# Optimization experiments

Measured on AMD Instinct MI355X. Metric: run time of the kernel, lower is better.

Reference implementation:

```python
import jax, jax.numpy as jnp
import numpy as np

B, S, D, H = 2, 2048, 1024, 16
HD = D // H  # head_dim = 64
SCALE = HD ** -0.5


def setup_inputs() -> dict:
    key = jax.random.key(0)
    k1, k2, k3 = jax.random.split(key, 3)
    src = jax.random.normal(k1, (B, S, D), dtype=jnp.float32)
    w_qkv = jax.random.normal(k2, (D, 3 * D), dtype=jnp.float32) * (D ** -0.5)
    b_qkv = jax.random.normal(k3, (3 * D,), dtype=jnp.float32) * 0.02
    return {"src": src, "w_qkv": w_qkv, "b_qkv": b_qkv}


def reference(src, w_qkv, b_qkv):
    # qkv projection: [B,S,3D]
    qkv = src @ w_qkv + b_qkv
    q, k, v = jnp.split(qkv, 3, axis=-1)
    # [B,S,D] -> [B,H,S,HD]
    def heads(x):
        return x.reshape(B, S, H, HD).transpose(0, 2, 1, 3)
    q, k, v = heads(q), heads(k), heads(v)
    # scaled dot-product attention (note: original scales AFTER q@k.T)
    attn = jnp.einsum('bhqd,bhkd->bhqk', q, k) * SCALE
    attn = jax.nn.softmax(attn, axis=-1)
    out = jnp.einsum('bhqk,bhkd->bhqd', attn, v)  # [B,H,S,HD]
    return out.transpose(0, 2, 1, 3).reshape(B, S, D)
```

## Files before the change

### kernel.cpp

```cpp
#include <hip/hip_runtime.h>
#include <hip/hip_bf16.h>

typedef short short8 __attribute__((ext_vector_type(8)));
typedef float f32x4 __attribute__((ext_vector_type(4)));
typedef float f32x16 __attribute__((ext_vector_type(16)));
typedef __hip_bfloat16 bf16;


__device__ __forceinline__ void glds16(const void* g, void* l) {
  __builtin_amdgcn_global_load_lds((const __attribute__((address_space(1))) unsigned int*)g,
                                   (__attribute__((address_space(3))) unsigned int*)l, 16, 0, 0);
}

__device__ __forceinline__ uint pk2(float a, float b) {
  union { bf16 h2[2]; uint u; } pk;
  pk.h2[0] = __float2bfloat16(a);
  pk.h2[1] = __float2bfloat16(b);
  return pk.u;
}

__global__ __launch_bounds__(256) void prep_kernel(const float4* __restrict__ in,
                                                   bf16* __restrict__ src_bf,
                                                   const float* __restrict__ w,
                                                   bf16* __restrict__ wt) {
  __shared__ float tile[32][33];
  const int bid = blockIdx.x;
  if (bid < 4096) {
    int i = bid * 256 + threadIdx.x;
    float4 v = in[i];
    union { bf16 h[4]; uint2 u; } pk;
    pk.h[0] = __float2bfloat16(v.x);
    pk.h[1] = __float2bfloat16(v.y);
    pk.h[2] = __float2bfloat16(v.z);
    pk.h[3] = __float2bfloat16(v.w);
    *(uint2*)(src_bf + (size_t)i * 4) = pk.u;
  } else {
    int id = bid - 4096;
    int x0 = (id % 96) * 32;
    int y0 = (id / 96) * 32;
    int tx = threadIdx.x & 31, ty = threadIdx.x >> 5;
#pragma unroll
    for (int i = 0; i < 4; i++) {
      int y = ty + i * 8;
      tile[y][tx] = w[(size_t)(y0 + y) * 3072 + x0 + tx];
    }
    __syncthreads();
#pragma unroll
    for (int i = 0; i < 4; i++) {
      int y = ty + i * 8;
      wt[(size_t)(x0 + y) * 1024 + y0 + tx] = __float2bfloat16(tile[tx][y]);
    }
  }
}

__global__ __launch_bounds__(256) void qkv_gemm_kernel(
    const bf16* __restrict__ A, const bf16* __restrict__ Bt,
    const float* __restrict__ bias,
    bf16* __restrict__ q_ws, bf16* __restrict__ k_ws, bf16* __restrict__ vt_ws) {
  __shared__ alignas(16) char AB[32768];
  const int tid = threadIdx.x;
  const int lane = tid & 63, wid = tid >> 6;
  const int lr = lane & 15, lg = lane >> 4;
  const int wm = wid >> 1, wn = wid & 1;
  const int m0 = blockIdx.x * 128, n0 = blockIdx.y * 128;

  const f32x4 z4 = {0.f, 0.f, 0.f, 0.f};
  f32x4 acc[4][4];
#pragma unroll
  for (int m = 0; m < 4; m++)
#pragma unroll
    for (int n = 0; n < 4; n++) acc[m][n] = z4;

  const int srow = lane >> 3;
  const int sseg = (lane & 7) ^ srow;
  const char* Ag = (const char*)A + (size_t)(m0 + wid * 32 + srow) * 2048 + sseg * 16;
  const char* Bg = (const char*)Bt + (size_t)(n0 + wid * 32 + srow) * 2048 + sseg * 16;
  char* Al = AB + wid * 4096;
  char* Bl = AB + 16384 + wid * 4096;
  const int xora = (lr & 7) << 4;

  for (int kt = 0; kt < 16; kt++) {
    __syncthreads();
#pragma unroll
    for (int c = 0; c < 4; c++) {
      glds16(Ag + (size_t)kt * 128 + c * 16384, Al + c * 1024);
      glds16(Bg + (size_t)kt * 128 + c * 16384, Bl + c * 1024);
    }
    asm volatile("s_waitcnt vmcnt(0)" ::: "memory");
    __syncthreads();
#pragma unroll
    for (int g = 0; g < 2; g++) {
      short8 af[4], bfr[4];
#pragma unroll
      for (int m = 0; m < 4; m++)
        af[m] = *(const short8*)(AB + (wm * 64 + m * 16 + lr) * 128 +
                                 ((g * 64 + lg * 16) ^ xora));
#pragma unroll
      for (int n = 0; n < 4; n++)
        bfr[n] = *(const short8*)(AB + 16384 + (wn * 64 + n * 16 + lr) * 128 +
                                  ((g * 64 + lg * 16) ^ xora));
#pragma unroll
      for (int m = 0; m < 4; m++)
#pragma unroll
        for (int n = 0; n < 4; n++)
          acc[m][n] = __builtin_amdgcn_mfma_f32_16x16x32_bf16(af[m], bfr[n], acc[m][n], 0, 0, 0);
    }
  }

  const int which = n0 >> 10;
#pragma unroll
  for (int m = 0; m < 4; m++) {
    int row = m0 + wm * 64 + m * 16 + lg * 4;
    int b = row >> 11;
    int ss0 = row & 2047;
#pragma unroll
    for (int n = 0; n < 4; n++) {
      int col = n0 + wn * 64 + n * 16 + lr;
      int d = col & 1023;
      int h = d >> 6, hd = d & 63;
      size_t bh = (size_t)(b * 16 + h);
      float bv = bias[col];
      if (which == 2) {
        union { bf16 h4[4]; uint2 u; } pk;
#pragma unroll
        for (int r = 0; r < 4; r++) pk.h4[r] = __float2bfloat16(acc[m][n][r] + bv);
        *(uint2*)&vt_ws[(bh * 64 + hd) * 2048 + ss0] = pk.u;
      } else {
        bf16* dst = (which == 0) ? q_ws : k_ws;
#pragma unroll
        for (int r = 0; r < 4; r++)
          dst[(bh * 2048 + (ss0 + r)) * 64 + hd] = __float2bfloat16(acc[m][n][r] + bv);
      }
    }
  }
}

__global__ __launch_bounds__(512) void attn6_kernel(
    const bf16* __restrict__ q_ws, const bf16* __restrict__ k_ws,
    const bf16* __restrict__ vt_ws, float* __restrict__ out) {
  __shared__ alignas(16) char smem[65536];
  const int tid = threadIdx.x;
  const int lane = tid & 63, wid = tid >> 6;
  const int lq = lane & 31, hi = lane >> 5;
  const int hi16 = hi * 16;
  const int xorv = (lq & 7) << 4;
  const float scale_l2e = 0.125f * 1.44269504088896f;

  const int f = blockIdx.x;
  const int bh = (f & 7) * 4 + ((f >> 3) & 3);
  const int qb = f >> 5;
  const int b = bh >> 4, h = bh & 15;
  const int q0 = qb * 256 + wid * 32;

  short8 qf[4];
  {
    const bf16* qrow = q_ws + ((size_t)bh * 2048 + q0 + lq) * 64;
#pragma unroll
    for (int s = 0; s < 4; s++) qf[s] = *(const short8*)(qrow + s * 16 + hi * 8);
  }

  const int l8 = lane >> 3;
  const int segk = (lane & 7) ^ l8;
  const char* kgl = (const char*)k_ws + (size_t)bh * 262144 +
                    (size_t)(wid * 16 + l8) * 128 + segk * 16;
  const int l16 = lane >> 4;
  const int d0v = (wid * 2 + 0) * 4 + l16;
  const int d1v = (wid * 2 + 1) * 4 + l16;
  const char* vg0 = (const char*)vt_ws + (size_t)bh * 262144 + (size_t)d0v * 4096 +
                    (((lane & 15) ^ (d0v & 15)) << 4);
  const char* vg1 = (const char*)vt_ws + (size_t)bh * 262144 + (size_t)d1v * 4096 +
                    (((lane & 15) ^ (d1v & 15)) << 4);

  f32x16 o0a, o0b, o1a, o1b, lacc;
#pragma unroll
  for (int r = 0; r < 16; r++) {
    o0a[r] = 0.f; o0b[r] = 0.f; o1a[r] = 0.f; o1b[r] = 0.f; lacc[r] = 0.f;
  }

  glds16(kgl, smem + wid * 2048);
  glds16(kgl + 1024, smem + wid * 2048 + 1024);
  glds16(vg0, smem + 32768 + wid * 2048);
  glds16(vg1, smem + 32768 + wid * 2048 + 1024);
  asm volatile("s_waitcnt vmcnt(0)" ::: "memory");
  __builtin_amdgcn_s_barrier();

  for (int kt = 0; kt < 16; ++kt) {
    const int kb_off = (kt & 1) * 16384;
    const int vb_off = 32768 + (kt & 1) * 16384;
    if (kt + 1 < 16) {
      const int nb = ((kt + 1) & 1) * 16384;
      glds16(kgl + (size_t)(kt + 1) * 16384, smem + nb + wid * 2048);
      glds16(kgl + (size_t)(kt + 1) * 16384 + 1024, smem + nb + wid * 2048 + 1024);
      glds16(vg0 + (size_t)(kt + 1) * 256, smem + 32768 + nb + wid * 2048);
      glds16(vg1 + (size_t)(kt + 1) * 256, smem + 32768 + nb + wid * 2048 + 1024);
    }

    f32x16 s0, s1, s2, s3;
#pragma unroll
    for (int r = 0; r < 16; r++) { s0[r] = 0.f; s1[r] = 0.f; s2[r] = 0.f; s3[r] = 0.f; }
#pragma unroll
    for (int st = 0; st < 4; st++) {
      const int doff = (st * 32 + hi16) ^ xorv;
      short8 ka = *(const short8*)(smem + kb_off + lq * 128 + doff);
      short8 kb = *(const short8*)(smem + kb_off + (lq + 32) * 128 + doff);
      short8 kc = *(const short8*)(smem + kb_off + (lq + 64) * 128 + doff);
      short8 kd = *(const short8*)(smem + kb_off + (lq + 96) * 128 + doff);
      __builtin_amdgcn_s_setprio(1);
      s0 = __builtin_amdgcn_mfma_f32_32x32x16_bf16(ka, qf[st], s0, 0, 0, 0);
      s1 = __builtin_amdgcn_mfma_f32_32x32x16_bf16(kb, qf[st], s1, 0, 0, 0);
      s2 = __builtin_amdgcn_mfma_f32_32x32x16_bf16(kc, qf[st], s2, 0, 0, 0);
      s3 = __builtin_amdgcn_mfma_f32_32x32x16_bf16(kd, qf[st], s3, 0, 0, 0);
      __builtin_amdgcn_s_setprio(0);
    }

#pragma unroll
    for (int r = 0; r < 16; r++) {
      s0[r] = __builtin_amdgcn_exp2f(s0[r] * scale_l2e);
      s1[r] = __builtin_amdgcn_exp2f(s1[r] * scale_l2e);
      s2[r] = __builtin_amdgcn_exp2f(s2[r] * scale_l2e);
      s3[r] = __builtin_amdgcn_exp2f(s3[r] * scale_l2e);
    }
#pragma unroll
    for (int r = 0; r < 16; r++)
      lacc[r] += (s0[r] + s1[r]) + (s2[r] + s3[r]);

#define PV_KB(S, KB, OA, OB)                                                     \
  {                                                                              \
    uint w0 = pk2(S[0], S[1]), w1 = pk2(S[2], S[3]);                             \
    uint w2 = pk2(S[4], S[5]), w3 = pk2(S[6], S[7]);                             \
    uint w4 = pk2(S[8], S[9]), w5 = pk2(S[10], S[11]);                           \
    uint w6 = pk2(S[12], S[13]), w7 = pk2(S[14], S[15]);                         \
    uint r0 = (uint)__shfl_xor((int)(hi ? w0 : w2), 32);                         \
    uint r1 = (uint)__shfl_xor((int)(hi ? w1 : w3), 32);                         \
    uint r2 = (uint)__shfl_xor((int)(hi ? w4 : w6), 32);                         \
    uint r3 = (uint)__shfl_xor((int)(hi ? w5 : w7), 32);                         \
    union { uint u[4]; short8 s8; } ua, ub;                                      \
    ua.u[0] = hi ? r0 : w0; ua.u[1] = hi ? r1 : w1;                              \
    ua.u[2] = hi ? w2 : r0; ua.u[3] = hi ? w3 : r1;                              \
    ub.u[0] = hi ? r2 : w4; ub.u[1] = hi ? r3 : w5;                              \
    ub.u[2] = hi ? w6 : r2; ub.u[3] = hi ? w7 : r3;                              \
    const int c0 = (((KB) * 4 + hi) ^ (lq & 15)) << 4;                           \
    const int c1 = (((KB) * 4 + 2 + hi) ^ (lq & 15)) << 4;                       \
    short8 va0 = *(const short8*)(smem + vb_off + lq * 256 + c0);                \
    short8 va1 = *(const short8*)(smem + vb_off + (lq + 32) * 256 + c0);         \
    short8 vb0 = *(const short8*)(smem + vb_off + lq * 256 + c1);                \
    short8 vb1 = *(const short8*)(smem + vb_off + (lq + 32) * 256 + c1);         \
    __builtin_amdgcn_s_setprio(1);                                               \
    OA = __builtin_amdgcn_mfma_f32_32x32x16_bf16(va0, ua.s8, OA, 0, 0, 0);       \
    OB = __builtin_amdgcn_mfma_f32_32x32x16_bf16(va1, ua.s8, OB, 0, 0, 0);       \
    OA = __builtin_amdgcn_mfma_f32_32x32x16_bf16(vb0, ub.s8, OA, 0, 0, 0);       \
    OB = __builtin_amdgcn_mfma_f32_32x32x16_bf16(vb1, ub.s8, OB, 0, 0, 0);       \
    __builtin_amdgcn_s_setprio(0);                                               \
  }
    PV_KB(s0, 0, o0a, o1a)
    PV_KB(s1, 1, o0b, o1b)
    PV_KB(s2, 2, o0a, o1a)
    PV_KB(s3, 3, o0b, o1b)
#undef PV_KB

    if (kt < 15) {
      asm volatile("s_waitcnt vmcnt(0)" ::: "memory");
      __builtin_amdgcn_s_barrier();
    }
  }
  __syncthreads();

  float l;
  {
    float sm[8];
#pragma unroll
    for (int i = 0; i < 8; i++) sm[i] = lacc[i] + lacc[i + 8];
#pragma unroll
    for (int i = 0; i < 4; i++) sm[i] += sm[i + 4];
    l = (sm[0] + sm[1]) + (sm[2] + sm[3]);
    l += __shfl_xor(l, 32);
  }
  f32x16 o0, o1;
#pragma unroll
  for (int r = 0; r < 16; r++) { o0[r] = o0a[r] + o0b[r]; o1[r] = o1a[r] + o1b[r]; }
  float* ep = (float*)(smem) + wid * 1024;
  const float invl = 1.f / l;
  const int eq = lane >> 1, eds = lane & 1;
  float* obase = out + ((size_t)b * 2048 + qb * 256 + wid * 32 + eq) * 1024 +
                 h * 64 + eds * 16;
#pragma unroll
  for (int db = 0; db < 2; db++) {
#pragma unroll
    for (int r = 0; r < 16; r++) {
      int d = (r & 3) + 8 * (r >> 2) + 4 * hi;
      float v = (db ? o1[r] : o0[r]) * invl;
      ep[lq * 32 + ((d + lq) & 31)] = v;
    }
#pragma unroll
    for (int c = 0; c < 4; c++) {
      float4 t;
      t.x = ep[eq * 32 + ((eds * 16 + 4 * c + 0 + eq) & 31)];
      t.y = ep[eq * 32 + ((eds * 16 + 4 * c + 1 + eq) & 31)];
      t.z = ep[eq * 32 + ((eds * 16 + 4 * c + 2 + eq) & 31)];
      t.w = ep[eq * 32 + ((eds * 16 + 4 * c + 3 + eq) & 31)];
      *(float4*)(obase + db * 32 + 4 * c) = t;
    }
  }
}

extern "C" void kernel_launch(void* const* d_in, const int* in_sizes, int n_in,
                              void* d_out, int out_size, void* d_ws, size_t ws_size,
                              hipStream_t stream) {
  (void)in_sizes; (void)n_in; (void)out_size; (void)ws_size;
  const float* src  = (const float*)d_in[0];
  const float* w    = (const float*)d_in[1];
  const float* bias = (const float*)d_in[2];
  float* out = (float*)d_out;

  char* ws = (char*)d_ws;
  bf16* src_bf = (bf16*)ws;
  bf16* wt_bf  = (bf16*)(ws + 8388608);
  bf16* q_ws   = (bf16*)(ws + 8388608 + 6291456);
  bf16* k_ws   = q_ws + 4194304;
  bf16* vt_ws  = k_ws + 4194304;

  prep_kernel<<<7168, 256, 0, stream>>>((const float4*)src, src_bf, w, wt_bf);
  qkv_gemm_kernel<<<dim3(32, 24), 256, 0, stream>>>(src_bf, wt_bf, bias, q_ws, k_ws, vt_ws);
  attn6_kernel<<<256, 512, 0, stream>>>(q_ws, k_ws, vt_ws, out);
}
```

Baseline: 96.78 us.

## Fold softmax scale into Q and permute K rows to drop P shuffles

Multiplies Q by scale*log2(e) in the QKV GEMM epilogue, so the attention kernel no longer multiplies each score before exp2. K rows are loaded into shared memory in a permuted order, which makes the S accumulator layout line up with the PV MFMA operand layout. That removes the cross-half lane shuffles and selects used when packing P. The scale is rounded into bf16 Q, which slightly changes precision, and the permutation must stay consistent with the V ordering.

```diff
diff --git a/kernel.cpp b/kernel.cpp
--- a/kernel.cpp
+++ b/kernel.cpp
@@ -108,6 +108,7 @@
   }
 
   const int which = n0 >> 10;
+  const float scl = (which == 0) ? 0.18033688f : 1.0f;
 #pragma unroll
   for (int m = 0; m < 4; m++) {
     int row = m0 + wm * 64 + m * 16 + lg * 4;
@@ -129,13 +130,16 @@
         bf16* dst = (which == 0) ? q_ws : k_ws;
 #pragma unroll
         for (int r = 0; r < 4; r++)
-          dst[(bh * 2048 + (ss0 + r)) * 64 + hd] = __float2bfloat16(acc[m][n][r] + bv);
+          dst[(bh * 2048 + (ss0 + r)) * 64 + hd] = __float2bfloat16((acc[m][n][r] + bv) * scl);
       }
     }
   }
 }
 
-__global__ __launch_bounds__(512) void attn6_kernel(
+#define KPERM(p) (((p) & ~31) | ((p) & 3) | ((((p) >> 2) & 1) << 3) | \
+                  ((((p) >> 3) & 1) << 4) | ((((p) >> 4) & 1) << 2))
+
+__global__ __launch_bounds__(512) void attn7_kernel(
     const bf16* __restrict__ q_ws, const bf16* __restrict__ k_ws,
     const bf16* __restrict__ vt_ws, float* __restrict__ out) {
   __shared__ alignas(16) char smem[65536];
@@ -144,7 +148,6 @@
   const int lq = lane & 31, hi = lane >> 5;
   const int hi16 = hi * 16;
   const int xorv = (lq & 7) << 4;
-  const float scale_l2e = 0.125f * 1.44269504088896f;
 
   const int f = blockIdx.x;
   const int bh = (f & 7) * 4 + ((f >> 3) & 3);
@@ -161,8 +164,12 @@
 
   const int l8 = lane >> 3;
   const int segk = (lane & 7) ^ l8;
-  const char* kgl = (const char*)k_ws + (size_t)bh * 262144 +
-                    (size_t)(wid * 16 + l8) * 128 + segk * 16;
+  const int p0 = wid * 16 + l8;
+  const int p1 = p0 + 8;
+  const char* kgl0 = (const char*)k_ws + (size_t)bh * 262144 +
+                     (size_t)KPERM(p0) * 128 + segk * 16;
+  const char* kgl1 = (const char*)k_ws + (size_t)bh * 262144 +
+                     (size_t)KPERM(p1) * 128 + segk * 16;
   const int l16 = lane >> 4;
   const int d0v = (wid * 2 + 0) * 4 + l16;
   const int d1v = (wid * 2 + 1) * 4 + l16;
@@ -177,8 +184,8 @@
     o0a[r] = 0.f; o0b[r] = 0.f; o1a[r] = 0.f; o1b[r] = 0.f; lacc[r] = 0.f;
   }
 
-  glds16(kgl, smem + wid * 2048);
-  glds16(kgl + 1024, smem + wid * 2048 + 1024);
+  glds16(kgl0, smem + wid * 2048);
+  glds16(kgl1, smem + wid * 2048 + 1024);
   glds16(vg0, smem + 32768 + wid * 2048);
   glds16(vg1, smem + 32768 + wid * 2048 + 1024);
   asm volatile("s_waitcnt vmcnt(0)" ::: "memory");
@@ -189,8 +196,8 @@
     const int vb_off = 32768 + (kt & 1) * 16384;
     if (kt + 1 < 16) {
       const int nb = ((kt + 1) & 1) * 16384;
-      glds16(kgl + (size_t)(kt + 1) * 16384, smem + nb + wid * 2048);
-      glds16(kgl + (size_t)(kt + 1) * 16384 + 1024, smem + nb + wid * 2048 + 1024);
+      glds16(kgl0 + (size_t)(kt + 1) * 16384, smem + nb + wid * 2048);
+      glds16(kgl1 + (size_t)(kt + 1) * 16384, smem + nb + wid * 2048 + 1024);
       glds16(vg0 + (size_t)(kt + 1) * 256, smem + 32768 + nb + wid * 2048);
       glds16(vg1 + (size_t)(kt + 1) * 256, smem + 32768 + nb + wid * 2048 + 1024);
     }
@@ -215,10 +222,10 @@
 
 #pragma unroll
     for (int r = 0; r < 16; r++) {
-      s0[r] = __builtin_amdgcn_exp2f(s0[r] * scale_l2e);
-      s1[r] = __builtin_amdgcn_exp2f(s1[r] * scale_l2e);
-      s2[r] = __builtin_amdgcn_exp2f(s2[r] * scale_l2e);
-      s3[r] = __builtin_amdgcn_exp2f(s3[r] * scale_l2e);
+      s0[r] = __builtin_amdgcn_exp2f(s0[r]);
+      s1[r] = __builtin_amdgcn_exp2f(s1[r]);
+      s2[r] = __builtin_amdgcn_exp2f(s2[r]);
+      s3[r] = __builtin_amdgcn_exp2f(s3[r]);
     }
 #pragma unroll
     for (int r = 0; r < 16; r++)
@@ -226,19 +233,11 @@
 
 #define PV_KB(S, KB, OA, OB)                                                     \
   {                                                                              \
-    uint w0 = pk2(S[0], S[1]), w1 = pk2(S[2], S[3]);                             \
-    uint w2 = pk2(S[4], S[5]), w3 = pk2(S[6], S[7]);                             \
-    uint w4 = pk2(S[8], S[9]), w5 = pk2(S[10], S[11]);                           \
-    uint w6 = pk2(S[12], S[13]), w7 = pk2(S[14], S[15]);                         \
-    uint r0 = (uint)__shfl_xor((int)(hi ? w0 : w2), 32);                         \
-    uint r1 = (uint)__shfl_xor((int)(hi ? w1 : w3), 32);                         \
-    uint r2 = (uint)__shfl_xor((int)(hi ? w4 : w6), 32);                         \
-    uint r3 = (uint)__shfl_xor((int)(hi ? w5 : w7), 32);                         \
     union { uint u[4]; short8 s8; } ua, ub;                                      \
-    ua.u[0] = hi ? r0 : w0; ua.u[1] = hi ? r1 : w1;                              \
-    ua.u[2] = hi ? w2 : r0; ua.u[3] = hi ? w3 : r1;                              \
-    ub.u[0] = hi ? r2 : w4; ub.u[1] = hi ? r3 : w5;                              \
-    ub.u[2] = hi ? w6 : r2; ub.u[3] = hi ? w7 : r3;                              \
+    ua.u[0] = pk2(S[0], S[1]);   ua.u[1] = pk2(S[2], S[3]);                      \
+    ua.u[2] = pk2(S[8], S[9]);   ua.u[3] = pk2(S[10], S[11]);                    \
+    ub.u[0] = pk2(S[4], S[5]);   ub.u[1] = pk2(S[6], S[7]);                      \
+    ub.u[2] = pk2(S[12], S[13]); ub.u[3] = pk2(S[14], S[15]);                    \
     const int c0 = (((KB) * 4 + hi) ^ (lq & 15)) << 4;                           \
     const int c1 = (((KB) * 4 + 2 + hi) ^ (lq & 15)) << 4;                       \
     short8 va0 = *(const short8*)(smem + vb_off + lq * 256 + c0);                \
@@ -321,5 +320,5 @@
 
   prep_kernel<<<7168, 256, 0, stream>>>((const float4*)src, src_bf, w, wt_bf);
   qkv_gemm_kernel<<<dim3(32, 24), 256, 0, stream>>>(src_bf, wt_bf, bias, q_ws, k_ws, vt_ws);
-  attn6_kernel<<<256, 512, 0, stream>>>(q_ws, k_ws, vt_ws, out);
-}
+  attn7_kernel<<<256, 512, 0, stream>>>(q_ws, k_ws, vt_ws, out);
+}
```

Result: faster. 90.22 us (-6.8%).
